# Optimization experiments

Hardware: AMD Instinct MI355X
Metric: run time of the kernel (lower is better)

Reference implementation:

```python
import jax, jax.numpy as jnp
from jax import lax
import numpy as np

DN = ('NCHW', 'OIHW', 'NCHW')

def conv2d(x, w, b, stride=1, padding=1):
    out = lax.conv_general_dilated(
        x, w, window_strides=(stride, stride),
        padding=[(padding, padding), (padding, padding)],
        dimension_numbers=DN)
    return out + b[None, :, None, None]

def maxpool2d(x, k=2, s=2):
    return lax.reduce_window(x, -jnp.inf, lax.max,
                             window_dimensions=(1, 1, k, k),
                             window_strides=(1, 1, s, s),
                             padding='VALID')

def setup_inputs() -> dict:
    key = jax.random.key(0)
    ks = jax.random.split(key, 9)
    B = 4096
    x = jax.random.normal(ks[0], (B, 3, 32, 32), dtype=jnp.float32)
    # weights initialized like torch.randn(...) * 0.1, biases zeros
    w1 = jax.random.normal(ks[1], (16, 3, 3, 3), dtype=jnp.float32) * 0.1
    b1 = jnp.zeros((16,), jnp.float32)
    w2 = jax.random.normal(ks[2], (32, 16, 3, 3), dtype=jnp.float32) * 0.1
    b2 = jnp.zeros((32,), jnp.float32)
    w3 = jax.random.normal(ks[3], (64, 32, 3, 3), dtype=jnp.float32) * 0.1
    b3 = jnp.zeros((64,), jnp.float32)
    # fc: Linear(64*4*4, 10); kaiming-uniform-ish init
    fan_in = 64 * 4 * 4
    bound = 1.0 / np.sqrt(fan_in)
    fc_w = jax.random.uniform(ks[4], (10, fan_in), jnp.float32, -bound, bound)
    fc_b = jax.random.uniform(ks[5], (10,), jnp.float32, -bound, bound)
    return {"x": x, "w1": w1, "b1": b1, "w2": w2, "b2": b2,
            "w3": w3, "b3": b3, "fc_w": fc_w, "fc_b": fc_b}

def reference(x, w1, b1, w2, b2, w3, b3, fc_w, fc_b):
    h = maxpool2d(jax.nn.relu(conv2d(x, w1, b1)))   # [B,16,16,16]
    h = maxpool2d(jax.nn.relu(conv2d(h, w2, b2)))   # [B,32,8,8]
    h = maxpool2d(jax.nn.relu(conv2d(h, w3, b3)))   # [B,64,4,4]
    h = h.reshape(h.shape[0], -1)                    # [B,1024]
    # dropout is identity in eval mode
    return h @ fc_w.T + fc_b
```

## Files before the change

### kernel.cpp

```cpp
#include <hip/hip_runtime.h>

typedef float f32x4 __attribute__((ext_vector_type(4)));
typedef float f32x16v __attribute__((ext_vector_type(16)));
typedef __bf16 bf16x4 __attribute__((ext_vector_type(4)));
typedef __bf16 bf16x8 __attribute__((ext_vector_type(8)));

#define B2P_OFF 0
#define B3P_OFF 9216
#define C1P_OFF 46080

__global__ __launch_bounds__(256) void pack_weights(
    const float* __restrict__ w1, const float* __restrict__ w2,
    const float* __restrict__ w3, __bf16* __restrict__ wsb) {
  int i = blockIdx.x * 256 + threadIdx.x;
  if (i < 9216) {
    int f = i >> 9, r = i & 511;
    int l = r >> 3, j = r & 7;
    int t = f >> 1, p = f & 1;
    int ky = t / 3, kx = t % 3;
    int oc = l & 31, ic = ((l >> 5) << 3) + j;
    float v = w2[oc * 144 + ic * 9 + ky * 3 + kx];
    __bf16 hi = (__bf16)v;
    wsb[B2P_OFF + i] = p ? (__bf16)(v - (float)hi) : hi;
  } else if (i < 9216 + 18432) {
    int q = i - 9216;
    int f = q >> 9, r = q & 511;
    int l = r >> 3, j = r & 7;
    int t = f >> 2, h = (f >> 1) & 1, nt = f & 1;
    int ky = t / 3, kx = t % 3;
    int oc = nt * 32 + (l & 31);
    int ic = h * 16 + ((l >> 5) << 3) + j;
    wsb[B3P_OFF + q] = (__bf16)w3[oc * 288 + ic * 9 + ky * 3 + kx];
  } else if (i >= 46080 && i < 47104) {
    int q = i - 46080;
    int f = q >> 9, r = q & 511;
    int l = r >> 3, j = r & 7;
    int oc = l & 15, kg = l >> 4;
    int half = j >> 2, ic = j & 3;
    float v = 0.f;
    if (ic < 3) {
      if (f == 0) {
        if (kg < 3)            v = w1[oc * 27 + ic * 9 + kg * 3 + half];
        else if (half == 0)    v = w1[oc * 27 + ic * 9 + 0 * 3 + 2];
      } else {
        if (half == 0 && kg < 2) v = w1[oc * 27 + ic * 9 + (kg + 1) * 3 + 2];
      }
    }
    wsb[C1P_OFF + q] = (__bf16)v;
  }
}

__global__ __launch_bounds__(256, 4) void cnn_fused(
    const float* __restrict__ x, const __bf16* __restrict__ wsb,
    const float* __restrict__ b1, const float* __restrict__ b2,
    const float* __restrict__ b3,
    const float* __restrict__ fcw, const float* __restrict__ fcb,
    float* __restrict__ out) {
  __shared__ __align__(16) unsigned char smem[27712];
  __bf16* s_img = (__bf16*)smem;
  __bf16* s2b   = (__bf16*)(smem + 9280);
  __bf16* s3b   = (__bf16*)smem;
  float*  h3s   = (float*)(smem + 9280);

  const __bf16* b2p = wsb + B2P_OFF;
  const __bf16* b3p = wsb + B3P_OFF;
  const __bf16* c1p = wsb + C1P_OFF;

  const int tid = threadIdx.x;
  const int img = blockIdx.x;
  const int w = tid >> 6, lane = tid & 63;

  if (tid < 132) {
    int row, col;
    if (tid < 34)       { row = 0;        col = tid; }
    else if (tid < 68)  { row = 33;       col = tid - 34; }
    else if (tid < 100) { row = tid - 67; col = 0; }
    else                { row = tid - 99; col = 33; }
    *(unsigned long long*)&s_img[(row * 34 + col) * 4] = 0ull;
  } else if (tid >= 248 && tid < 252) {
    *(unsigned long long*)&s_img[4624 + (tid - 248) * 4] = 0ull;
  }
  {
    const float* xg = x + img * 3072;
    const int r = tid * 4;
    const int y = r >> 5, xx = r & 31;
    const f32x4 c0 = *(const f32x4*)&xg[r];
    const f32x4 c1 = *(const f32x4*)&xg[r + 1024];
    const f32x4 c2 = *(const f32x4*)&xg[r + 2048];
    bf16x4 pk[4];
    #pragma unroll
    for (int k = 0; k < 4; ++k) {
      pk[k].x = (__bf16)c0[k];
      pk[k].y = (__bf16)c1[k];
      pk[k].z = (__bf16)c2[k];
      pk[k].w = (__bf16)0.f;
    }
    const int base = ((y + 1) * 34 + (xx + 1)) * 4;
    __builtin_memcpy(&s_img[base],     &pk[0], 16);
    __builtin_memcpy(&s_img[base + 8], &pk[2], 16);
  }
  const bf16x8 B1h = *(const bf16x8*)(c1p + lane * 8);
  const bf16x8 B2h = *(const bf16x8*)(c1p + 512 + lane * 8);
  __syncthreads();

  float pooled[16];
  {
    const int xm = lane & 15, kg = lane >> 4;
    const int d1r = (kg == 3) ? 0 : kg;
    const int d1c = (kg == 3) ? 2 : 0;
    const int d2r = (kg == 0) ? 1 : 2;
    const int dd1 = d1r * 34 + d1c;
    const int dd2 = d2r * 34 + 2;
    #pragma unroll
    for (int p = 0; p < 4; ++p) {
      f32x4 acc[2][2];
      #pragma unroll
      for (int ys = 0; ys < 2; ++ys)
        #pragma unroll
        for (int xh = 0; xh < 2; ++xh)
          #pragma unroll
          for (int r = 0; r < 4; ++r) acc[ys][xh][r] = 0.f;
      #pragma unroll
      for (int ys = 0; ys < 2; ++ys) {
        const int yqg = w * 8 + p * 2 + ys;
        #pragma unroll
        for (int xh = 0; xh < 2; ++xh) {
          const int cb = yqg * 34 + xh * 16 + xm;
          bf16x8 A1, A2;
          __builtin_memcpy(&A1, &s_img[(cb + dd1) * 4], 16);
          __builtin_memcpy(&A2, &s_img[(cb + dd2) * 4], 16);
          acc[ys][xh] = __builtin_amdgcn_mfma_f32_16x16x32_bf16(A1, B1h, acc[ys][xh], 0, 0, 0);
          acc[ys][xh] = __builtin_amdgcn_mfma_f32_16x16x32_bf16(A2, B2h, acc[ys][xh], 0, 0, 0);
        }
      }
      #pragma unroll
      for (int xh = 0; xh < 2; ++xh)
        #pragma unroll
        for (int xp2 = 0; xp2 < 2; ++xp2) {
          const float v0 = fmaxf(acc[0][xh][xp2 * 2], acc[0][xh][xp2 * 2 + 1]);
          const float v1 = fmaxf(acc[1][xh][xp2 * 2], acc[1][xh][xp2 * 2 + 1]);
          pooled[p * 4 + xh * 2 + xp2] = fmaxf(v0, v1);
        }
    }
  }

  if (tid < 68) {
    int row, col;
    if (tid < 18)      { row = 0;       col = tid; }
    else if (tid < 36) { row = 17;      col = tid - 18; }
    else if (tid < 52) { row = tid - 35; col = 0; }
    else               { row = tid - 51; col = 17; }
    unsigned long long* p = (unsigned long long*)&s2b[row * 512 + col * 28];
    #pragma unroll
    for (int u = 0; u < 7; ++u) p[u] = 0ull;
  }
  {
    const int oc = lane & 15, quad = lane >> 4;
    const float bias = b1[oc];
    #pragma unroll
    for (int p = 0; p < 4; ++p)
      #pragma unroll
      for (int xh = 0; xh < 2; ++xh)
        #pragma unroll
        for (int xp2 = 0; xp2 < 2; ++xp2) {
          const float v = fmaxf(pooled[p * 4 + xh * 2 + xp2] + bias, 0.f);
          const int py = w * 4 + p, px = xh * 8 + quad * 2 + xp2;
          s2b[(py + 1) * 512 + (px + 1) * 28 + oc] = (__bf16)v;
        }
  }
  bf16x8 Bf[9];
  #pragma unroll
  for (int t = 0; t < 9; ++t)
    Bf[t] = *(const bf16x8*)(b2p + (t * 2) * 512 + lane * 8);
  __syncthreads();

  float pooled2[8];
  {
    const unsigned short* s2 = (const unsigned short*)s2b;
    const int xm = lane & 15, yoff = (lane >> 4) & 1, kh = lane >> 5;
    f32x16v acc0, acc1;
    #pragma unroll
    for (int r = 0; r < 16; ++r) { acc0[r] = 0.f; acc1[r] = 0.f; }
    const int rb0 = (4 * w + yoff) * 512;
    const int rb1 = rb0 + 2 * 512;
    #pragma unroll
    for (int t = 0; t < 9; ++t) {
      const int ky = t / 3, kx = t % 3;
      const int ro = ky * 512 + (xm + kx) * 28 + kh * 8;
      bf16x8 a0, a1;
      __builtin_memcpy(&a0, &s2[rb0 + ro], 16);
      __builtin_memcpy(&a1, &s2[rb1 + ro], 16);
      acc0 = __builtin_amdgcn_mfma_f32_32x32x16_bf16(a0, Bf[t], acc0, 0, 0, 0);
      acc1 = __builtin_amdgcn_mfma_f32_32x32x16_bf16(a1, Bf[t], acc1, 0, 0, 0);
    }
    #pragma unroll
    for (int bq = 0; bq < 2; ++bq)
      #pragma unroll
      for (int rq = 0; rq < 2; ++rq) {
        const int r0 = bq * 4 + rq * 2;
        pooled2[bq * 2 + rq] =
            fmaxf(fmaxf(acc0[r0], acc0[r0 + 1]), fmaxf(acc0[r0 + 8], acc0[r0 + 9]));
        pooled2[4 + bq * 2 + rq] =
            fmaxf(fmaxf(acc1[r0], acc1[r0 + 1]), fmaxf(acc1[r0 + 8], acc1[r0 + 9]));
      }
  }

  if (tid < 36) {
    int row, col;
    if (tid < 10)      { row = 0;       col = tid; }
    else if (tid < 20) { row = 9;       col = tid - 10; }
    else if (tid < 28) { row = tid - 19; col = 0; }
    else               { row = tid - 27; col = 9; }
    unsigned long long* p = (unsigned long long*)&s3b[row * 448 + col * 40];
    #pragma unroll
    for (int u = 0; u < 8; ++u) p[u] = 0ull;
  }
  {
    const int oc = lane & 31, hh = lane >> 5;
    const float bias = b2[oc];
    #pragma unroll
    for (int i2 = 0; i2 < 2; ++i2)
      #pragma unroll
      for (int bq = 0; bq < 2; ++bq)
        #pragma unroll
        for (int rq = 0; rq < 2; ++rq) {
          const float v = fmaxf(pooled2[i2 * 4 + bq * 2 + rq] + bias, 0.f);
          const int py = 2 * w + i2, px = 2 * hh + 4 * bq + rq;
          s3b[(py + 1) * 448 + (px + 1) * 40 + oc] = (__bf16)v;
        }
  }
  __syncthreads();

  {
    const unsigned short* s3 = (const unsigned short*)s3b;
    const int mtile = w >> 1, ntile = w & 1;
    bf16x8 Bt[18];
    #pragma unroll
    for (int t = 0; t < 9; ++t)
      #pragma unroll
      for (int h = 0; h < 2; ++h)
        Bt[t * 2 + h] = *(const bf16x8*)(b3p + (t * 4 + h * 2 + ntile) * 512 + lane * 8);
    const int m = lane & 31, half = lane >> 5;
    const int py = m >> 3, px = m & 7;
    f32x16v accA, accB;
    #pragma unroll
    for (int r = 0; r < 16; ++r) { accA[r] = 0.f; accB[r] = 0.f; }
    #pragma unroll
    for (int t = 0; t < 9; ++t) {
      const int ky = t / 3, kx = t % 3;
      const int ro = (mtile * 4 + py + ky) * 448 + (px + kx) * 40 + half * 8;
      bf16x8 a0 = *(const bf16x8*)&s3[ro];
      bf16x8 a1 = *(const bf16x8*)&s3[ro + 16];
      accA = __builtin_amdgcn_mfma_f32_32x32x16_bf16(a0, Bt[t * 2 + 0], accA, 0, 0, 0);
      accB = __builtin_amdgcn_mfma_f32_32x32x16_bf16(a1, Bt[t * 2 + 1], accB, 0, 0, 0);
    }
    const int oc = ntile * 32 + (lane & 31);
    const float bias = b3[oc];
    #pragma unroll
    for (int i = 0; i < 2; ++i)
      #pragma unroll
      for (int jq = 0; jq < 2; ++jq) {
        const int r0 = 8 * i + 2 * jq;
        const float s00 = accA[r0]     + accB[r0];
        const float s01 = accA[r0 + 1] + accB[r0 + 1];
        const float s10 = accA[r0 + 4] + accB[r0 + 4];
        const float s11 = accA[r0 + 5] + accB[r0 + 5];
        const float v = fmaxf(fmaxf(s00, s01), fmaxf(s10, s11));
        const int gy = mtile * 2 + i, gx = 2 * half + jq;
        h3s[oc * 20 + gy * 4 + gx] = fmaxf(v + bias, 0.f);
      }
  }
  __syncthreads();

  {
    f32x4 hv[4];
    #pragma unroll
    for (int k = 0; k < 4; ++k) hv[k] = *(const f32x4*)&h3s[lane * 20 + k * 4];
    f32x4 fw[3][4];
    float bv[3];
    #pragma unroll
    for (int jj = 0; jj < 3; ++jj) {
      const int j = w + jj * 4;
      const int js = (j < 10) ? j : 0;
      const f32x4* fw4 = (const f32x4*)&fcw[js * 1024 + lane * 16];
      #pragma unroll
      for (int k = 0; k < 4; ++k) fw[jj][k] = fw4[k];
      bv[jj] = fcb[js];
    }
    float dot[3] = {0.f, 0.f, 0.f};
    #pragma unroll
    for (int k = 0; k < 4; ++k)
      #pragma unroll
      for (int jj = 0; jj < 3; ++jj) {
        dot[jj] = fmaf(hv[k][0], fw[jj][k][0], dot[jj]);
        dot[jj] = fmaf(hv[k][1], fw[jj][k][1], dot[jj]);
        dot[jj] = fmaf(hv[k][2], fw[jj][k][2], dot[jj]);
        dot[jj] = fmaf(hv[k][3], fw[jj][k][3], dot[jj]);
      }
    #pragma unroll
    for (int s = 32; s > 0; s >>= 1)
      #pragma unroll
      for (int jj = 0; jj < 3; ++jj)
        dot[jj] += __shfl_xor(dot[jj], s, 64);
    if (lane == 0) {
      #pragma unroll
      for (int jj = 0; jj < 3; ++jj) {
        const int j = w + jj * 4;
        if (j < 10) out[img * 10 + j] = dot[jj] + bv[jj];
      }
    }
  }
}

extern "C" void kernel_launch(void* const* d_in, const int* in_sizes, int n_in,
                              void* d_out, int out_size, void* d_ws, size_t ws_size,
                              hipStream_t stream) {
  const float* x   = (const float*)d_in[0];
  const float* w1  = (const float*)d_in[1];
  const float* b1  = (const float*)d_in[2];
  const float* w2  = (const float*)d_in[3];
  const float* b2  = (const float*)d_in[4];
  const float* w3  = (const float*)d_in[5];
  const float* b3  = (const float*)d_in[6];
  const float* fcw = (const float*)d_in[7];
  const float* fcb = (const float*)d_in[8];
  __bf16* wsb = (__bf16*)d_ws;
  float* out = (float*)d_out;

  hipLaunchKernelGGL(pack_weights, dim3(184), dim3(256), 0, stream, w1, w2, w3, wsb);
  hipLaunchKernelGGL(cnn_fused, dim3(4096), dim3(256), 0, stream,
                     x, wsb, b1, b2, b3, fcw, fcb, out);
}
```

Baseline: 128.1 us.

## Recast conv1 as 32x32x16 MFMA with direct pooled store to shared

Conv1 weights are repacked into three K=16 slices, one per kernel row, and conv1 now runs as three 32x32x16 bf16 MFMAs per tile instead of pairs of 16x16x32 MFMAs. Max-pool, bias and ReLU are applied in the accumulator and written straight to shared memory, with no intermediate pooled register array. The border zeroing moves before the only barrier, which removes one __syncthreads. In exchange, half of the 32 output columns (oc 16-31) are zero padding, so each tile does more matrix work while issuing fewer LDS loads.

```diff
diff --git a/kernel.cpp b/kernel.cpp
--- a/kernel.cpp
+++ b/kernel.cpp
@@ -31,21 +31,17 @@
     int oc = nt * 32 + (l & 31);
     int ic = h * 16 + ((l >> 5) << 3) + j;
     wsb[B3P_OFF + q] = (__bf16)w3[oc * 288 + ic * 9 + ky * 3 + kx];
-  } else if (i >= 46080 && i < 47104) {
+  } else if (i >= 46080 && i < 46080 + 1536) {
     int q = i - 46080;
-    int f = q >> 9, r = q & 511;
+    int f = q >> 9;
+    int r = q & 511;
     int l = r >> 3, j = r & 7;
-    int oc = l & 15, kg = l >> 4;
-    int half = j >> 2, ic = j & 3;
+    int k = ((l >> 5) << 3) + j;
+    int kx = k >> 2, ic = k & 3;
+    int ocn = l & 31;
     float v = 0.f;
-    if (ic < 3) {
-      if (f == 0) {
-        if (kg < 3)            v = w1[oc * 27 + ic * 9 + kg * 3 + half];
-        else if (half == 0)    v = w1[oc * 27 + ic * 9 + 0 * 3 + 2];
-      } else {
-        if (half == 0 && kg < 2) v = w1[oc * 27 + ic * 9 + (kg + 1) * 3 + 2];
-      }
-    }
+    if (ocn < 16 && ic < 3 && kx < 3)
+      v = w1[ocn * 27 + ic * 9 + f * 3 + kx];
     wsb[C1P_OFF + q] = (__bf16)v;
   }
 }
@@ -99,51 +95,9 @@
     __builtin_memcpy(&s_img[base],     &pk[0], 16);
     __builtin_memcpy(&s_img[base + 8], &pk[2], 16);
   }
-  const bf16x8 B1h = *(const bf16x8*)(c1p + lane * 8);
-  const bf16x8 B2h = *(const bf16x8*)(c1p + 512 + lane * 8);
-  __syncthreads();
-
-  float pooled[16];
-  {
-    const int xm = lane & 15, kg = lane >> 4;
-    const int d1r = (kg == 3) ? 0 : kg;
-    const int d1c = (kg == 3) ? 2 : 0;
-    const int d2r = (kg == 0) ? 1 : 2;
-    const int dd1 = d1r * 34 + d1c;
-    const int dd2 = d2r * 34 + 2;
-    #pragma unroll
-    for (int p = 0; p < 4; ++p) {
-      f32x4 acc[2][2];
-      #pragma unroll
-      for (int ys = 0; ys < 2; ++ys)
-        #pragma unroll
-        for (int xh = 0; xh < 2; ++xh)
-          #pragma unroll
-          for (int r = 0; r < 4; ++r) acc[ys][xh][r] = 0.f;
-      #pragma unroll
-      for (int ys = 0; ys < 2; ++ys) {
-        const int yqg = w * 8 + p * 2 + ys;
-        #pragma unroll
-        for (int xh = 0; xh < 2; ++xh) {
-          const int cb = yqg * 34 + xh * 16 + xm;
-          bf16x8 A1, A2;
-          __builtin_memcpy(&A1, &s_img[(cb + dd1) * 4], 16);
-          __builtin_memcpy(&A2, &s_img[(cb + dd2) * 4], 16);
-          acc[ys][xh] = __builtin_amdgcn_mfma_f32_16x16x32_bf16(A1, B1h, acc[ys][xh], 0, 0, 0);
-          acc[ys][xh] = __builtin_amdgcn_mfma_f32_16x16x32_bf16(A2, B2h, acc[ys][xh], 0, 0, 0);
-        }
-      }
-      #pragma unroll
-      for (int xh = 0; xh < 2; ++xh)
-        #pragma unroll
-        for (int xp2 = 0; xp2 < 2; ++xp2) {
-          const float v0 = fmaxf(acc[0][xh][xp2 * 2], acc[0][xh][xp2 * 2 + 1]);
-          const float v1 = fmaxf(acc[1][xh][xp2 * 2], acc[1][xh][xp2 * 2 + 1]);
-          pooled[p * 4 + xh * 2 + xp2] = fmaxf(v0, v1);
-        }
-    }
-  }
-
+  const bf16x8 Bc0 = *(const bf16x8*)(c1p + 0 * 512 + lane * 8);
+  const bf16x8 Bc1 = *(const bf16x8*)(c1p + 1 * 512 + lane * 8);
+  const bf16x8 Bc2 = *(const bf16x8*)(c1p + 2 * 512 + lane * 8);
   if (tid < 68) {
     int row, col;
     if (tid < 18)      { row = 0;       col = tid; }
@@ -154,19 +108,43 @@
     #pragma unroll
     for (int u = 0; u < 7; ++u) p[u] = 0ull;
   }
-  {
-    const int oc = lane & 15, quad = lane >> 4;
-    const float bias = b1[oc];
-    #pragma unroll
-    for (int p = 0; p < 4; ++p)
-      #pragma unroll
-      for (int xh = 0; xh < 2; ++xh)
+  __syncthreads();
+
+  {
+    const int m = lane & 31, half = lane >> 5;
+    const int yoff = m >> 4, xm = m & 15;
+    const bool store = (m < 16);
+    const float bias = b1[m & 15];
+    #pragma unroll
+    for (int i1 = 0; i1 < 4; ++i1) {
+      #pragma unroll
+      for (int xh = 0; xh < 2; ++xh) {
+        f32x16v acc;
         #pragma unroll
-        for (int xp2 = 0; xp2 < 2; ++xp2) {
-          const float v = fmaxf(pooled[p * 4 + xh * 2 + xp2] + bias, 0.f);
-          const int py = w * 4 + p, px = xh * 8 + quad * 2 + xp2;
-          s2b[(py + 1) * 512 + (px + 1) * 28 + oc] = (__bf16)v;
+        for (int r = 0; r < 16; ++r) acc[r] = 0.f;
+        const int arow = 8 * w + 2 * i1 + yoff;
+        const int acol = xh * 16 + xm + half * 2;
+        bf16x8 A0, A1, A2;
+        __builtin_memcpy(&A0, &s_img[((arow + 0) * 34 + acol) * 4], 16);
+        __builtin_memcpy(&A1, &s_img[((arow + 1) * 34 + acol) * 4], 16);
+        __builtin_memcpy(&A2, &s_img[((arow + 2) * 34 + acol) * 4], 16);
+        acc = __builtin_amdgcn_mfma_f32_32x32x16_bf16(A0, Bc0, acc, 0, 0, 0);
+        acc = __builtin_amdgcn_mfma_f32_32x32x16_bf16(A1, Bc1, acc, 0, 0, 0);
+        acc = __builtin_amdgcn_mfma_f32_32x32x16_bf16(A2, Bc2, acc, 0, 0, 0);
+        if (store) {
+          #pragma unroll
+          for (int qi = 0; qi < 4; ++qi) {
+            const int rb = (qi & 1) * 2 + (qi >> 1) * 4;
+            float v = fmaxf(fmaxf(acc[rb], acc[rb + 1]),
+                            fmaxf(acc[rb + 8], acc[rb + 9]));
+            v = fmaxf(v + bias, 0.f);
+            const int q = half * 2 + (qi & 1) + (qi >> 1) * 4;
+            const int py = 4 * w + i1, px = xh * 8 + q;
+            s2b[(py + 1) * 512 + (px + 1) * 28 + m] = (__bf16)v;
+          }
         }
+      }
+    }
   }
   bf16x8 Bf[9];
   #pragma unroll
@@ -327,7 +305,7 @@
   __bf16* wsb = (__bf16*)d_ws;
   float* out = (float*)d_out;
 
-  hipLaunchKernelGGL(pack_weights, dim3(184), dim3(256), 0, stream, w1, w2, w3, wsb);
+  hipLaunchKernelGGL(pack_weights, dim3(186), dim3(256), 0, stream, w1, w2, w3, wsb);
   hipLaunchKernelGGL(cnn_fused, dim3(4096), dim3(256), 0, stream,
                      x, wsb, b1, b2, b3, fcw, fcb, out);
 }
```

New measurement: 131.6 us. 1.03x slower.
